# Kernel optimization log

Hardware: AMD Instinct MI355X
Metric: run time of the kernel (lower is better)

## Reference

```python
import jax, jax.numpy as jnp
import numpy as np

D_MODEL = 1024
NUM_HEADS = 16
HEAD_DIM = D_MODEL // NUM_HEADS
MAX_SEQ = 512


def rope_tables(seq_len, dim):
    inv_freq = 1.0 / (10000.0 ** (jnp.arange(0, dim, 2, dtype=jnp.float32) / dim))
    t = jnp.arange(seq_len, dtype=jnp.float32)
    freqs = jnp.einsum('i,j->ij', t, inv_freq)        # [S, dim/2]
    emb = jnp.concatenate([freqs, freqs], axis=-1)    # [S, dim]
    return jnp.cos(emb), jnp.sin(emb)


def rotate_half(x):
    x1, x2 = jnp.split(x, 2, axis=-1)
    return jnp.concatenate([-x2, x1], axis=-1)


def setup_inputs() -> dict:
    key = jax.random.key(0)
    ks = jax.random.split(key, 12)
    B, S, D = 16, 512, D_MODEL
    s = 1.0 / np.sqrt(D)
    inp = {
        'query': jax.random.normal(ks[0], (B, S, D), jnp.float32),
        'key': jax.random.normal(ks[1], (B, S, D), jnp.float32),
        'value': jax.random.normal(ks[2], (B, S, D), jnp.float32),
        'Wq': jax.random.normal(ks[3], (D, D), jnp.float32) * s,
        'bq': jnp.zeros((D,), jnp.float32),
        'Wk': jax.random.normal(ks[4], (D, D), jnp.float32) * s,
        'bk': jnp.zeros((D,), jnp.float32),
        'Wv': jax.random.normal(ks[5], (D, D), jnp.float32) * s,
        'bv': jnp.zeros((D,), jnp.float32),
        'Wo': jax.random.normal(ks[6], (D, D), jnp.float32) * s,
        'bo': jnp.zeros((D,), jnp.float32),
    }
    return inp


def reference(query, key, value, Wq, bq, Wk, bk, Wv, bv, Wo, bo):
    B, S, D = query.shape
    H, Hd = NUM_HEADS, HEAD_DIM
    scale = Hd ** -0.5

    def proj(x, W, b):  # torch Linear: x @ W.T + b -> [B,H,S,Hd]
        y = jnp.einsum('bsd,ed->bse', x, W) + b
        return y.reshape(B, S, H, Hd).transpose(0, 2, 1, 3)

    q = proj(query, Wq, bq)
    k = proj(key, Wk, bk)
    v = proj(value, Wv, bv)

    cos, sin = rope_tables(S, Hd)           # [S, Hd]
    cos = cos[None, None]                    # [1,1,S,Hd]
    sin = sin[None, None]
    q = q * cos + rotate_half(q) * sin
    k = k * cos + rotate_half(k) * sin

    attn = jnp.einsum('bhqd,bhkd->bhqk', q, k) * scale
    attn_w = jax.nn.softmax(attn, axis=-1)
    out = jnp.einsum('bhqk,bhkd->bhqd', attn_w, v)
    out = out.transpose(0, 2, 1, 3).reshape(B, S, D)
    out = jnp.einsum('bsd,ed->bse', out, Wo) + bo
    return out
```

## Files before the change

kernel.cpp:

```cpp
#include <hip/hip_runtime.h>
#include <hip/hip_bf16.h>
#include <math.h>

typedef __attribute__((ext_vector_type(8))) short short8;
typedef __attribute__((ext_vector_type(4))) float f32x4;
typedef unsigned short ushort;
typedef unsigned int uint;

#define BATCH 16
#define SEQ 512
#define DMODEL 1024
#define NHEADS 16
#define HD 64
#define MTOT (BATCH * SEQ)
#define NBUF ((size_t)MTOT * DMODEL)
#define WBUF ((size_t)DMODEL * DMODEL)

__device__ __forceinline__ ushort f2bf(float f) {
    union { float f; uint i; } v; v.f = f;
    uint r = v.i + 0x7fffu + ((v.i >> 16) & 1u);
    return (ushort)(r >> 16);
}

__device__ __forceinline__ short8 cvt8(float4 a, float4 b) {
    short8 r;
    r[0] = (short)f2bf(a.x); r[1] = (short)f2bf(a.y);
    r[2] = (short)f2bf(a.z); r[3] = (short)f2bf(a.w);
    r[4] = (short)f2bf(b.x); r[5] = (short)f2bf(b.y);
    r[6] = (short)f2bf(b.z); r[7] = (short)f2bf(b.w);
    return r;
}

__device__ __forceinline__ void gld16(const ushort* g, ushort* l) {
    __builtin_amdgcn_global_load_lds(
        (const __attribute__((address_space(1))) void*)g,
        (__attribute__((address_space(3))) void*)l, 16, 0, 0);
}

__device__ __forceinline__ f32x4 mfma16(short8 a, short8 b, f32x4 c) {
    return __builtin_amdgcn_mfma_f32_16x16x32_bf16(a, b, c, 0, 0, 0);
}

__global__ void fill_const(float* __restrict__ out, float val) {
    out[blockIdx.x * 256 + threadIdx.x] = val;
}

__global__ __launch_bounds__(256) void cvt_act(
    const float* __restrict__ i0, const float* __restrict__ i1,
    const float* __restrict__ i2, ushort* __restrict__ o0,
    ushort* __restrict__ o1, ushort* __restrict__ o2)
{
    const float* in  = blockIdx.y == 0 ? i0 : (blockIdx.y == 1 ? i1 : i2);
    ushort*      out = blockIdx.y == 0 ? o0 : (blockIdx.y == 1 ? o1 : o2);
    int i = (blockIdx.x * 256 + threadIdx.x) * 8;
    float4 a = *(const float4*)(in + i);
    float4 b = *(const float4*)(in + i + 4);
    *(short8*)(out + i) = cvt8(a, b);
}

__global__ __launch_bounds__(256) void cvt_w(
    const float* __restrict__ i0, const float* __restrict__ i1,
    const float* __restrict__ i2, const float* __restrict__ i3,
    ushort* __restrict__ o0, ushort* __restrict__ o1,
    ushort* __restrict__ o2, ushort* __restrict__ o3)
{
    const float* in  = blockIdx.y == 0 ? i0 : (blockIdx.y == 1 ? i1 :
                        (blockIdx.y == 2 ? i2 : i3));
    ushort*      out = blockIdx.y == 0 ? o0 : (blockIdx.y == 1 ? o1 :
                        (blockIdx.y == 2 ? o2 : o3));
    int i = (blockIdx.x * 256 + threadIdx.x) * 8;
    float4 a = *(const float4*)(in + i);
    float4 b = *(const float4*)(in + i + 4);
    *(short8*)(out + i) = cvt8(a, b);
}

__global__ void rope_init(float* __restrict__ cs, float* __restrict__ sn) {
    int idx = blockIdx.x * 256 + threadIdx.x;
    if (idx >= SEQ * 32) return;
    int s = idx >> 5, p = idx & 31;
    float inv = __expf(-(float)p * (1.0f / 32.0f) * logf(10000.0f));
    float th = (float)s * inv;
    cs[idx] = cosf(th);
    sn[idx] = sinf(th);
}

__global__ __launch_bounds__(256) void qkv_proj(
    const ushort* __restrict__ Aq, const ushort* __restrict__ Ak,
    const ushort* __restrict__ Av, const ushort* __restrict__ Wq,
    const ushort* __restrict__ Wk, const ushort* __restrict__ Wv,
    const float* __restrict__ bq, const float* __restrict__ bk,
    const float* __restrict__ bv, ushort* __restrict__ Qo,
    ushort* __restrict__ Ko, ushort* __restrict__ Vo,
    const float* __restrict__ cs_tab, const float* __restrict__ sn_tab)
{
    const int z = blockIdx.z;
    const ushort* A    = z == 0 ? Aq : (z == 1 ? Ak : Av);
    const ushort* W    = z == 0 ? Wq : (z == 1 ? Wk : Wv);
    const float*  bias = z == 0 ? bq : (z == 1 ? bk : bv);
    ushort*       out  = z == 0 ? Qo : (z == 1 ? Ko : Vo);

    const int id = blockIdx.x;
    const int j8 = id >> 3;
    const int by = (id & 7) * 8 + (j8 & 7);
    const int bx = j8 >> 3;

    __shared__ ushort sA[128 * 32];
    __shared__ ushort sB[128 * 32];
    const int tid = threadIdx.x;
    const int wave = tid >> 6, lane = tid & 63;
    const int quad = lane >> 4, l16 = lane & 15;
    const int m0 = by * 128, n0 = bx * 128;
    const int wm = (wave >> 1) * 64, wn = (wave & 1) * 64;

    f32x4 acc[4][4] = {};

    const int c0 = tid, c1 = tid + 256;
    const int r0 = c0 >> 2, k0c = (c0 & 3) * 8;
    const int r1 = c1 >> 2, k1c = (c1 & 3) * 8;
    const ushort* A0 = A + (size_t)(m0 + r0) * 1024 + k0c;
    const ushort* A1 = A + (size_t)(m0 + r1) * 1024 + k1c;
    const ushort* B0 = W + (size_t)(n0 + r0) * 1024 + k0c;
    const ushort* B1 = W + (size_t)(n0 + r1) * 1024 + k1c;

    for (int k = 0; k < 1024; k += 32) {
        gld16(A0 + k, sA + c0 * 8);
        gld16(A1 + k, sA + c1 * 8);
        gld16(B0 + k, sB + c0 * 8);
        gld16(B1 + k, sB + c1 * 8);
        __syncthreads();

        short8 af[4], bf[4];
#pragma unroll
        for (int i = 0; i < 4; i++) {
            af[i] = *(const short8*)(sA + (wm + i * 16 + l16) * 32 + quad * 8);
            bf[i] = *(const short8*)(sB + (wn + i * 16 + l16) * 32 + quad * 8);
        }
#pragma unroll
        for (int i = 0; i < 4; i++)
#pragma unroll
            for (int j = 0; j < 4; j++)
                acc[i][j] = mfma16(af[i], bf[j], acc[i][j]);
        __syncthreads();
    }

    float bv4[4];
#pragma unroll
    for (int j = 0; j < 4; j++) bv4[j] = bias[n0 + wn + j * 16 + l16];

    if (z < 2) {
        const int h = (n0 + wn) >> 6;
#pragma unroll
        for (int i = 0; i < 4; i++) {
#pragma unroll
            for (int r = 0; r < 4; r++) {
                int m = m0 + wm + i * 16 + quad * 4 + r;
                int s = m & (SEQ - 1), b = m >> 9;
                size_t base = ((size_t)(b * NHEADS + h) * SEQ + s) * HD;
#pragma unroll
                for (int jj = 0; jj < 2; jj++) {
                    int p = jj * 16 + l16;
                    float c = cs_tab[s * 32 + p], sg = sn_tab[s * 32 + p];
                    float lo = acc[i][jj][r] + bv4[jj];
                    float hi = acc[i][jj + 2][r] + bv4[jj + 2];
                    out[base + p]      = f2bf(lo * c - hi * sg);
                    out[base + 32 + p] = f2bf(hi * c + lo * sg);
                }
            }
        }
    } else {
#pragma unroll
        for (int i = 0; i < 4; i++)
#pragma unroll
            for (int jj = 0; jj < 4; jj++) {
                int n = n0 + wn + jj * 16 + l16;
                int h = n >> 6, d = n & 63;
#pragma unroll
                for (int r = 0; r < 4; r++) {
                    int m = m0 + wm + i * 16 + quad * 4 + r;
                    int s = m & (SEQ - 1), b = m >> 9;
                    out[((size_t)(b * NHEADS + h) * HD + d) * SEQ + s] =
                        f2bf(acc[i][jj][r] + bv4[jj]);
                }
            }
    }
}

__global__ __launch_bounds__(256) void gemm_o(
    const ushort* __restrict__ A, const ushort* __restrict__ W,
    const float* __restrict__ bias, float* __restrict__ out)
{
    const int id = blockIdx.x;
    const int j8 = id >> 3;
    const int by = (id & 7) * 8 + (j8 & 7);
    const int bx = j8 >> 3;

    __shared__ ushort sA[128 * 32];
    __shared__ ushort sB[128 * 32];
    const int tid = threadIdx.x;
    const int wave = tid >> 6, lane = tid & 63;
    const int quad = lane >> 4, l16 = lane & 15;
    const int m0 = by * 128, n0 = bx * 128;
    const int wm = (wave >> 1) * 64, wn = (wave & 1) * 64;

    f32x4 acc[4][4] = {};

    const int c0 = tid, c1 = tid + 256;
    const int r0 = c0 >> 2, k0c = (c0 & 3) * 8;
    const int r1 = c1 >> 2, k1c = (c1 & 3) * 8;
    const ushort* A0 = A + (size_t)(m0 + r0) * 1024 + k0c;
    const ushort* A1 = A + (size_t)(m0 + r1) * 1024 + k1c;
    const ushort* B0 = W + (size_t)(n0 + r0) * 1024 + k0c;
    const ushort* B1 = W + (size_t)(n0 + r1) * 1024 + k1c;

    for (int k = 0; k < 1024; k += 32) {
        gld16(A0 + k, sA + c0 * 8);
        gld16(A1 + k, sA + c1 * 8);
        gld16(B0 + k, sB + c0 * 8);
        gld16(B1 + k, sB + c1 * 8);
        __syncthreads();

        short8 af[4], bf[4];
#pragma unroll
        for (int i = 0; i < 4; i++) {
            af[i] = *(const short8*)(sA + (wm + i * 16 + l16) * 32 + quad * 8);
            bf[i] = *(const short8*)(sB + (wn + i * 16 + l16) * 32 + quad * 8);
        }
#pragma unroll
        for (int i = 0; i < 4; i++)
#pragma unroll
            for (int j = 0; j < 4; j++)
                acc[i][j] = mfma16(af[i], bf[j], acc[i][j]);
        __syncthreads();
    }

    float bv4[4];
#pragma unroll
    for (int j = 0; j < 4; j++) bv4[j] = bias[n0 + wn + j * 16 + l16];

#pragma unroll
    for (int i = 0; i < 4; i++)
#pragma unroll
        for (int j = 0; j < 4; j++) {
            int n = n0 + wn + j * 16 + l16;
#pragma unroll
            for (int r = 0; r < 4; r++) {
                int m = m0 + wm + i * 16 + quad * 4 + r;
                out[(size_t)m * 1024 + n] = acc[i][j][r] + bv4[j];
            }
        }
}

__global__ __launch_bounds__(256) void attn(
    const ushort* __restrict__ Q, const ushort* __restrict__ K,
    const ushort* __restrict__ VT, ushort* __restrict__ O)
{
    __shared__ ushort sK[64 * 64];
    __shared__ ushort sV[64 * 64];
    __shared__ ushort sP[4][32 * 72];

    const int tid = threadIdx.x;
    const int wave = tid >> 6, lane = tid & 63;
    const int quad = lane >> 4, l16 = lane & 15;
    const int id = blockIdx.x;
    const int j8 = id >> 3;
    const int bh = (id & 7) * 32 + (j8 >> 2);
    const int q0 = (j8 & 3) * 128;
    const int qw = q0 + wave * 32;

    const ushort* Qbh = Q + (size_t)bh * SEQ * HD;
    const ushort* Kbh = K + (size_t)bh * SEQ * HD;
    const ushort* Vbh = VT + (size_t)bh * HD * SEQ;

    const float S2 = 0.125f * 1.44269504f;
    const float C2 = 12.0f * 1.44269504f;

    short8 qf[2][2];
#pragma unroll
    for (int mi = 0; mi < 2; mi++)
#pragma unroll
        for (int ks = 0; ks < 2; ks++)
            qf[mi][ks] = *(const short8*)(Qbh + (size_t)(qw + mi * 16 + l16) * HD +
                                          ks * 32 + quad * 8);

    f32x4 o_acc[2][4] = {};
    float lsum[2][4] = {};

    const int cA = tid, cB = tid + 256;
    const int rA = cA >> 3, colA = (cA & 7) * 8;
    const int rB = cB >> 3, colB = (cB & 7) * 8;

    for (int kt = 0; kt < SEQ; kt += 64) {
        *(short8*)(sK + cA * 8) = *(const short8*)(Kbh + (size_t)(kt + rA) * HD + colA);
        *(short8*)(sK + cB * 8) = *(const short8*)(Kbh + (size_t)(kt + rB) * HD + colB);
        *(short8*)(sV + cA * 8) = *(const short8*)(Vbh + (size_t)rA * SEQ + kt + colA);
        *(short8*)(sV + cB * 8) = *(const short8*)(Vbh + (size_t)rB * SEQ + kt + colB);
        __syncthreads();

        f32x4 sc[2][4];
#pragma unroll
        for (int nj = 0; nj < 4; nj++) {
            short8 kf0 = *(const short8*)(sK + (nj * 16 + l16) * 64 + quad * 8);
            short8 kf1 = *(const short8*)(sK + (nj * 16 + l16) * 64 + 32 + quad * 8);
#pragma unroll
            for (int mi = 0; mi < 2; mi++) {
                f32x4 z = {0.f, 0.f, 0.f, 0.f};
                z = mfma16(qf[mi][0], kf0, z);
                z = mfma16(qf[mi][1], kf1, z);
                sc[mi][nj] = z;
            }
        }

#pragma unroll
        for (int mi = 0; mi < 2; mi++)
#pragma unroll
            for (int r = 0; r < 4; r++) {
                float p0 = __builtin_amdgcn_exp2f(fmaf(sc[mi][0][r], S2, -C2));
                float p1 = __builtin_amdgcn_exp2f(fmaf(sc[mi][1][r], S2, -C2));
                float p2 = __builtin_amdgcn_exp2f(fmaf(sc[mi][2][r], S2, -C2));
                float p3 = __builtin_amdgcn_exp2f(fmaf(sc[mi][3][r], S2, -C2));
                sc[mi][0][r] = p0; sc[mi][1][r] = p1;
                sc[mi][2][r] = p2; sc[mi][3][r] = p3;
                lsum[mi][r] += (p0 + p1) + (p2 + p3);
            }

#pragma unroll
        for (int mi = 0; mi < 2; mi++)
#pragma unroll
            for (int nj = 0; nj < 4; nj++)
#pragma unroll
                for (int r = 0; r < 4; r++)
                    sP[wave][(mi * 16 + quad * 4 + r) * 72 + nj * 16 + l16] =
                        f2bf(sc[mi][nj][r]);
        __syncthreads();

#pragma unroll
        for (int ks = 0; ks < 2; ks++) {
            short8 pf0 = *(const short8*)(&sP[wave][(l16) * 72 + ks * 32 + quad * 8]);
            short8 pf1 = *(const short8*)(&sP[wave][(16 + l16) * 72 + ks * 32 + quad * 8]);
#pragma unroll
            for (int dj = 0; dj < 4; dj++) {
                short8 vf = *(const short8*)(sV + (dj * 16 + l16) * 64 + ks * 32 + quad * 8);
                o_acc[0][dj] = mfma16(pf0, vf, o_acc[0][dj]);
                o_acc[1][dj] = mfma16(pf1, vf, o_acc[1][dj]);
            }
        }
        __syncthreads();
    }

    const int h = bh & (NHEADS - 1), b = bh >> 4;
#pragma unroll
    for (int mi = 0; mi < 2; mi++)
#pragma unroll
        for (int r = 0; r < 4; r++) {
            float l = lsum[mi][r];
            l += __shfl_xor(l, 1, 64);
            l += __shfl_xor(l, 2, 64);
            l += __shfl_xor(l, 4, 64);
            l += __shfl_xor(l, 8, 64);
            float inv = 1.0f / l;
            int s = qw + mi * 16 + quad * 4 + r;
            size_t base = ((size_t)(b * SEQ + s)) * DMODEL + h * HD;
#pragma unroll
            for (int dj = 0; dj < 4; dj++)
                O[base + dj * 16 + l16] = f2bf(o_acc[mi][dj][r] * inv);
        }
}

extern "C" void kernel_launch(void* const* d_in, const int* in_sizes, int n_in,
                              void* d_out, int out_size, void* d_ws, size_t ws_size,
                              hipStream_t stream) {
    bool ok = (n_in == 11) && (out_size == (int)NBUF) &&
              in_sizes[0] == (int)NBUF && in_sizes[1] == (int)NBUF &&
              in_sizes[2] == (int)NBUF &&
              in_sizes[3] == (int)WBUF && in_sizes[4] == 1024 &&
              in_sizes[5] == (int)WBUF && in_sizes[6] == 1024 &&
              in_sizes[7] == (int)WBUF && in_sizes[8] == 1024 &&
              in_sizes[9] == (int)WBUF && in_sizes[10] == 1024;
    if (!ok) {
        fill_const<<<NBUF / 256, 256, 0, stream>>>((float*)d_out, 1000.0f);
        return;
    }
    size_t need = 2 * (size_t)SEQ * 32 * 4 + 4 * NBUF * 2 + 4 * WBUF * 2;
    if (ws_size < need) return;

    const float* q  = (const float*)d_in[0];
    const float* k  = (const float*)d_in[1];
    const float* v  = (const float*)d_in[2];
    const float* Wq = (const float*)d_in[3];
    const float* bq = (const float*)d_in[4];
    const float* Wk = (const float*)d_in[5];
    const float* bk = (const float*)d_in[6];
    const float* Wv = (const float*)d_in[7];
    const float* bv = (const float*)d_in[8];
    const float* Wo = (const float*)d_in[9];
    const float* bo = (const float*)d_in[10];

    float* cs = (float*)d_ws;
    float* sn = cs + SEQ * 32;
    ushort* Qb  = (ushort*)(sn + SEQ * 32);
    ushort* Kb  = Qb + NBUF;
    ushort* VTb = Kb + NBUF;
    ushort* Xb  = VTb + NBUF;
    ushort* Wqb = Xb + NBUF;
    ushort* Wkb = Wqb + WBUF;
    ushort* Wvb = Wkb + WBUF;
    ushort* Wob = Wvb + WBUF;
    ushort* Qx = (ushort*)d_out;
    ushort* Kx = Qx + NBUF;

    rope_init<<<64, 256, 0, stream>>>(cs, sn);
    cvt_w<<<dim3(WBUF / 2048, 4), 256, 0, stream>>>(Wq, Wk, Wv, Wo,
                                                    Wqb, Wkb, Wvb, Wob);
    cvt_act<<<dim3(NBUF / 2048, 3), 256, 0, stream>>>(q, k, v, Qx, Kx, Xb);

    qkv_proj<<<dim3(512, 1, 3), 256, 0, stream>>>(
        Qx, Kx, Xb, Wqb, Wkb, Wvb, bq, bk, bv, Qb, Kb, VTb, cs, sn);

    attn<<<BATCH * NHEADS * 4, 256, 0, stream>>>(Qb, Kb, VTb, Xb);

    gemm_o<<<512, 256, 0, stream>>>(Xb, Wob, bo, (float*)d_out);
}
```

Baseline: 313.4 us.

## Rewrite GEMM mainloop with 256x128 tiles, triple-buffered async loads and XOR swizzle

Replaces the simple double-sync GEMM loop in qkv_proj and gemm_o with a shared mainloop using 256x128 block tiles, 512 threads, BK=64, and a three-stage LDS ring fed by global_load_lds. Explicit vmcnt waits and split barriers let the loads overlap the MFMA work, and setprio favours the math phase. An XOR swizzle on LDS columns is meant to avoid bank conflicts. Separately, the attention kernel pads its K and V LDS rows to 72 elements to reduce bank conflicts. The risks are heavier LDS use and lower occupancy, and the hand-written waitcnt logic must stay correct.

```diff
diff --git a/kernel.cpp b/kernel.cpp
--- a/kernel.cpp
+++ b/kernel.cpp
@@ -16,6 +16,9 @@
 #define NBUF ((size_t)MTOT * DMODEL)
 #define WBUF ((size_t)DMODEL * DMODEL)
 
+#define SZA (256 * 64)
+#define SZB (128 * 64)
+
 __device__ __forceinline__ ushort f2bf(float f) {
     union { float f; uint i; } v; v.f = f;
     uint r = v.i + 0x7fffu + ((v.i >> 16) & 1u);
@@ -84,7 +87,108 @@
     sn[idx] = sinf(th);
 }
 
-__global__ __launch_bounds__(256) void qkv_proj(
+__device__ __forceinline__ void gemm_main(
+    const ushort* __restrict__ A, const ushort* __restrict__ W,
+    ushort* smA, ushort* smB, int m0, int n0, int tid, f32x4 (&acc)[4][4])
+{
+    const int lane = tid & 63, w = tid >> 6;
+    const int quad = lane >> 4, l16 = lane & 15;
+    const int wm = (w >> 1) * 64, wn = (w & 1) * 64;
+
+    const int rA  = tid >> 3;
+    const int kcs = ((tid & 7) ^ (rA & 7)) * 8;
+    const ushort* gA = A + (size_t)(m0 + rA) * 1024 + kcs;
+    const ushort* gB = W + (size_t)(n0 + rA) * 1024 + kcs;
+    ushort* lA = smA + tid * 8;
+    ushort* lB = smB + tid * 8;
+
+    const int swz = (l16 & 7) << 3;
+    const int k0 = (quad * 8) ^ swz;
+    const int k1 = (32 + quad * 8) ^ swz;
+
+#pragma unroll
+    for (int i = 0; i < 4; ++i) gld16(gA + i * 65536,      lA + i * 4096);
+#pragma unroll
+    for (int i = 0; i < 2; ++i) gld16(gB + i * 65536,      lB + i * 4096);
+#pragma unroll
+    for (int i = 0; i < 4; ++i) gld16(gA + i * 65536 + 64, lA + SZA + i * 4096);
+#pragma unroll
+    for (int i = 0; i < 2; ++i) gld16(gB + i * 65536 + 64, lB + SZB + i * 4096);
+
+    int bc = 0, bs = 2;
+    short8 af[2][2], bf[4][2];
+
+#pragma unroll 1
+    for (int t = 0; t < 16; ++t) {
+        if (t == 15) asm volatile("s_waitcnt vmcnt(0)" ::: "memory");
+        else         asm volatile("s_waitcnt vmcnt(6)" ::: "memory");
+        __builtin_amdgcn_s_barrier();
+
+        const ushort* tA = smA + bc * SZA;
+        const ushort* tB = smB + bc * SZB;
+        const bool st = t < 14;
+        const int koff = (t + 2) * 64;
+
+#pragma unroll
+        for (int mi = 0; mi < 2; ++mi) {
+            const ushort* r = tA + (wm + mi * 16 + l16) * 64;
+            af[mi][0] = *(const short8*)(r + k0);
+            af[mi][1] = *(const short8*)(r + k1);
+        }
+#pragma unroll
+        for (int nj = 0; nj < 4; ++nj) {
+            const ushort* r = tB + (wn + nj * 16 + l16) * 64;
+            bf[nj][0] = *(const short8*)(r + k0);
+            bf[nj][1] = *(const short8*)(r + k1);
+        }
+        if (st) {
+            gld16(gA + 0 * 65536 + koff, lA + bs * SZA + 0 * 4096);
+            gld16(gA + 1 * 65536 + koff, lA + bs * SZA + 1 * 4096);
+            gld16(gB + 0 * 65536 + koff, lB + bs * SZB + 0 * 4096);
+        }
+        __builtin_amdgcn_s_barrier();
+        asm volatile("s_waitcnt lgkmcnt(0)" ::: "memory");
+        __builtin_amdgcn_s_setprio(1);
+#pragma unroll
+        for (int nj = 0; nj < 4; ++nj)
+#pragma unroll
+            for (int mi = 0; mi < 2; ++mi) {
+                acc[mi][nj] = mfma16(af[mi][0], bf[nj][0], acc[mi][nj]);
+                acc[mi][nj] = mfma16(af[mi][1], bf[nj][1], acc[mi][nj]);
+            }
+        __builtin_amdgcn_s_setprio(0);
+        __builtin_amdgcn_s_barrier();
+
+#pragma unroll
+        for (int mi = 0; mi < 2; ++mi) {
+            const ushort* r = tA + (wm + (2 + mi) * 16 + l16) * 64;
+            af[mi][0] = *(const short8*)(r + k0);
+            af[mi][1] = *(const short8*)(r + k1);
+        }
+        if (st) {
+            gld16(gA + 2 * 65536 + koff, lA + bs * SZA + 2 * 4096);
+            gld16(gA + 3 * 65536 + koff, lA + bs * SZA + 3 * 4096);
+            gld16(gB + 1 * 65536 + koff, lB + bs * SZB + 1 * 4096);
+        }
+        __builtin_amdgcn_s_barrier();
+        asm volatile("s_waitcnt lgkmcnt(0)" ::: "memory");
+        __builtin_amdgcn_s_setprio(1);
+#pragma unroll
+        for (int nj = 0; nj < 4; ++nj)
+#pragma unroll
+            for (int mi = 0; mi < 2; ++mi) {
+                acc[2 + mi][nj] = mfma16(af[mi][0], bf[nj][0], acc[2 + mi][nj]);
+                acc[2 + mi][nj] = mfma16(af[mi][1], bf[nj][1], acc[2 + mi][nj]);
+            }
+        __builtin_amdgcn_s_setprio(0);
+        __builtin_amdgcn_s_barrier();
+
+        bc = bc == 2 ? 0 : bc + 1;
+        bs = bs == 2 ? 0 : bs + 1;
+    }
+}
+
+__global__ __launch_bounds__(512) void qkv_proj(
     const ushort* __restrict__ Aq, const ushort* __restrict__ Ak,
     const ushort* __restrict__ Av, const ushort* __restrict__ Wq,
     const ushort* __restrict__ Wk, const ushort* __restrict__ Wv,
@@ -100,48 +204,21 @@
     ushort*       out  = z == 0 ? Qo : (z == 1 ? Ko : Vo);
 
     const int id = blockIdx.x;
-    const int j8 = id >> 3;
-    const int by = (id & 7) * 8 + (j8 & 7);
-    const int bx = j8 >> 3;
-
-    __shared__ ushort sA[128 * 32];
-    __shared__ ushort sB[128 * 32];
+    const int x = id & 7, l = id >> 3;
+    const int by = x * 4 + (l >> 3);
+    const int bx = l & 7;
+    const int m0 = by * 256, n0 = bx * 128;
+
+    __shared__ __align__(16) ushort smA[3 * SZA];
+    __shared__ __align__(16) ushort smB[3 * SZB];
+
     const int tid = threadIdx.x;
-    const int wave = tid >> 6, lane = tid & 63;
+    const int lane = tid & 63, w = tid >> 6;
     const int quad = lane >> 4, l16 = lane & 15;
-    const int m0 = by * 128, n0 = bx * 128;
-    const int wm = (wave >> 1) * 64, wn = (wave & 1) * 64;
+    const int wm = (w >> 1) * 64, wn = (w & 1) * 64;
 
     f32x4 acc[4][4] = {};
-
-    const int c0 = tid, c1 = tid + 256;
-    const int r0 = c0 >> 2, k0c = (c0 & 3) * 8;
-    const int r1 = c1 >> 2, k1c = (c1 & 3) * 8;
-    const ushort* A0 = A + (size_t)(m0 + r0) * 1024 + k0c;
-    const ushort* A1 = A + (size_t)(m0 + r1) * 1024 + k1c;
-    const ushort* B0 = W + (size_t)(n0 + r0) * 1024 + k0c;
-    const ushort* B1 = W + (size_t)(n0 + r1) * 1024 + k1c;
-
-    for (int k = 0; k < 1024; k += 32) {
-        gld16(A0 + k, sA + c0 * 8);
-        gld16(A1 + k, sA + c1 * 8);
-        gld16(B0 + k, sB + c0 * 8);
-        gld16(B1 + k, sB + c1 * 8);
-        __syncthreads();
-
-        short8 af[4], bf[4];
-#pragma unroll
-        for (int i = 0; i < 4; i++) {
-            af[i] = *(const short8*)(sA + (wm + i * 16 + l16) * 32 + quad * 8);
-            bf[i] = *(const short8*)(sB + (wn + i * 16 + l16) * 32 + quad * 8);
-        }
-#pragma unroll
-        for (int i = 0; i < 4; i++)
-#pragma unroll
-            for (int j = 0; j < 4; j++)
-                acc[i][j] = mfma16(af[i], bf[j], acc[i][j]);
-        __syncthreads();
-    }
+    gemm_main(A, W, smA, smB, m0, n0, tid, acc);
 
     float bv4[4];
 #pragma unroll
@@ -185,53 +262,26 @@
     }
 }
 
-__global__ __launch_bounds__(256) void gemm_o(
+__global__ __launch_bounds__(512) void gemm_o(
     const ushort* __restrict__ A, const ushort* __restrict__ W,
     const float* __restrict__ bias, float* __restrict__ out)
 {
     const int id = blockIdx.x;
-    const int j8 = id >> 3;
-    const int by = (id & 7) * 8 + (j8 & 7);
-    const int bx = j8 >> 3;
-
-    __shared__ ushort sA[128 * 32];
-    __shared__ ushort sB[128 * 32];
+    const int x = id & 7, l = id >> 3;
+    const int by = x * 4 + (l >> 3);
+    const int bx = l & 7;
+    const int m0 = by * 256, n0 = bx * 128;
+
+    __shared__ __align__(16) ushort smA[3 * SZA];
+    __shared__ __align__(16) ushort smB[3 * SZB];
+
     const int tid = threadIdx.x;
-    const int wave = tid >> 6, lane = tid & 63;
+    const int lane = tid & 63, w = tid >> 6;
     const int quad = lane >> 4, l16 = lane & 15;
-    const int m0 = by * 128, n0 = bx * 128;
-    const int wm = (wave >> 1) * 64, wn = (wave & 1) * 64;
+    const int wm = (w >> 1) * 64, wn = (w & 1) * 64;
 
     f32x4 acc[4][4] = {};
-
-    const int c0 = tid, c1 = tid + 256;
-    const int r0 = c0 >> 2, k0c = (c0 & 3) * 8;
-    const int r1 = c1 >> 2, k1c = (c1 & 3) * 8;
-    const ushort* A0 = A + (size_t)(m0 + r0) * 1024 + k0c;
-    const ushort* A1 = A + (size_t)(m0 + r1) * 1024 + k1c;
-    const ushort* B0 = W + (size_t)(n0 + r0) * 1024 + k0c;
-    const ushort* B1 = W + (size_t)(n0 + r1) * 1024 + k1c;
-
-    for (int k = 0; k < 1024; k += 32) {
-        gld16(A0 + k, sA + c0 * 8);
-        gld16(A1 + k, sA + c1 * 8);
-        gld16(B0 + k, sB + c0 * 8);
-        gld16(B1 + k, sB + c1 * 8);
-        __syncthreads();
-
-        short8 af[4], bf[4];
-#pragma unroll
-        for (int i = 0; i < 4; i++) {
-            af[i] = *(const short8*)(sA + (wm + i * 16 + l16) * 32 + quad * 8);
-            bf[i] = *(const short8*)(sB + (wn + i * 16 + l16) * 32 + quad * 8);
-        }
-#pragma unroll
-        for (int i = 0; i < 4; i++)
-#pragma unroll
-            for (int j = 0; j < 4; j++)
-                acc[i][j] = mfma16(af[i], bf[j], acc[i][j]);
-        __syncthreads();
-    }
+    gemm_main(A, W, smA, smB, m0, n0, tid, acc);
 
     float bv4[4];
 #pragma unroll
@@ -254,8 +304,8 @@
     const ushort* __restrict__ Q, const ushort* __restrict__ K,
     const ushort* __restrict__ VT, ushort* __restrict__ O)
 {
-    __shared__ ushort sK[64 * 64];
-    __shared__ ushort sV[64 * 64];
+    __shared__ ushort sK[64 * 72];
+    __shared__ ushort sV[64 * 72];
     __shared__ ushort sP[4][32 * 72];
 
     const int tid = threadIdx.x;
@@ -290,17 +340,17 @@
     const int rB = cB >> 3, colB = (cB & 7) * 8;
 
     for (int kt = 0; kt < SEQ; kt += 64) {
-        *(short8*)(sK + cA * 8) = *(const short8*)(Kbh + (size_t)(kt + rA) * HD + colA);
-        *(short8*)(sK + cB * 8) = *(const short8*)(Kbh + (size_t)(kt + rB) * HD + colB);
-        *(short8*)(sV + cA * 8) = *(const short8*)(Vbh + (size_t)rA * SEQ + kt + colA);
-        *(short8*)(sV + cB * 8) = *(const short8*)(Vbh + (size_t)rB * SEQ + kt + colB);
+        *(short8*)(sK + rA * 72 + colA) = *(const short8*)(Kbh + (size_t)(kt + rA) * HD + colA);
+        *(short8*)(sK + rB * 72 + colB) = *(const short8*)(Kbh + (size_t)(kt + rB) * HD + colB);
+        *(short8*)(sV + rA * 72 + colA) = *(const short8*)(Vbh + (size_t)rA * SEQ + kt + colA);
+        *(short8*)(sV + rB * 72 + colB) = *(const short8*)(Vbh + (size_t)rB * SEQ + kt + colB);
         __syncthreads();
 
         f32x4 sc[2][4];
 #pragma unroll
         for (int nj = 0; nj < 4; nj++) {
-            short8 kf0 = *(const short8*)(sK + (nj * 16 + l16) * 64 + quad * 8);
-            short8 kf1 = *(const short8*)(sK + (nj * 16 + l16) * 64 + 32 + quad * 8);
+            short8 kf0 = *(const short8*)(sK + (nj * 16 + l16) * 72 + quad * 8);
+            short8 kf1 = *(const short8*)(sK + (nj * 16 + l16) * 72 + 32 + quad * 8);
 #pragma unroll
             for (int mi = 0; mi < 2; mi++) {
                 f32x4 z = {0.f, 0.f, 0.f, 0.f};
@@ -339,7 +389,7 @@
             short8 pf1 = *(const short8*)(&sP[wave][(16 + l16) * 72 + ks * 32 + quad * 8]);
 #pragma unroll
             for (int dj = 0; dj < 4; dj++) {
-                short8 vf = *(const short8*)(sV + (dj * 16 + l16) * 64 + ks * 32 + quad * 8);
+                short8 vf = *(const short8*)(sV + (dj * 16 + l16) * 72 + ks * 32 + quad * 8);
                 o_acc[0][dj] = mfma16(pf0, vf, o_acc[0][dj]);
                 o_acc[1][dj] = mfma16(pf1, vf, o_acc[1][dj]);
             }
@@ -413,10 +463,10 @@
                                                     Wqb, Wkb, Wvb, Wob);
     cvt_act<<<dim3(NBUF / 2048, 3), 256, 0, stream>>>(q, k, v, Qx, Kx, Xb);
 
-    qkv_proj<<<dim3(512, 1, 3), 256, 0, stream>>>(
+    qkv_proj<<<dim3(256, 1, 3), 512, 0, stream>>>(
         Qx, Kx, Xb, Wqb, Wkb, Wvb, bq, bk, bv, Qb, Kb, VTb, cs, sn);
 
     attn<<<BATCH * NHEADS * 4, 256, 0, stream>>>(Qb, Kb, VTb, Xb);
 
-    gemm_o<<<512, 256, 0, stream>>>(Xb, Wob, bo, (float*)d_out);
-}
+    gemm_o<<<256, 512, 0, stream>>>(Xb, Wob, bo, (float*)d_out);
+}
```

After: 294.6 us. -6.0%, faster.
